# Optimization experiments

Hardware: AMD Instinct MI355X
Metric: run time of the kernel (lower is better)

Reference implementation:

```python
import jax, jax.numpy as jnp
import numpy as np
import math

D_MODEL = 1024
N_HEAD = 16
Q_DIM = K_DIM = V_DIM = 1024
SCALE = math.sqrt(D_MODEL // N_HEAD)  # 8.0
B, LQ, LK = 2, 2048, 2048


def setup_inputs() -> dict:
    key = jax.random.key(0)
    ks = jax.random.split(key, 10)
    s = 1.0 / math.sqrt(Q_DIM)
    return {
        "q": jax.random.normal(ks[0], (B, LQ, Q_DIM), jnp.float32),
        "k": jax.random.normal(ks[1], (B, LK, K_DIM), jnp.float32),
        "v": jax.random.normal(ks[2], (B, LK, V_DIM), jnp.float32),
        "mask": jax.random.randint(ks[3], (B, LQ, LK), 0, 2, jnp.int32),
        "Wq": jax.random.uniform(ks[4], (D_MODEL, Q_DIM), jnp.float32, -s, s),
        "bq": jnp.zeros((D_MODEL,), jnp.float32),
        "Wk": jax.random.uniform(ks[5], (D_MODEL, K_DIM), jnp.float32, -s, s),
        "bk": jnp.zeros((D_MODEL,), jnp.float32),
        "Wv": jax.random.uniform(ks[6], (D_MODEL, V_DIM), jnp.float32, -s, s),
        "bv": jnp.zeros((D_MODEL,), jnp.float32),
    }


def reference(q, k, v, Wq, bq, Wk, bk, Wv, bv, mask):
    b, lq, _ = q.shape
    lk = k.shape[1]
    dh = D_MODEL // N_HEAD
    # linear projections (torch Linear: x @ W.T + b)
    qh = (q @ Wq.T + bq).reshape(b, lq, N_HEAD, dh).transpose(0, 2, 1, 3)  # bhqd
    kh = (k @ Wk.T + bk).reshape(b, lk, N_HEAD, dh).transpose(0, 2, 1, 3)  # bhkd
    vh = (v @ Wv.T + bv).reshape(b, lk, N_HEAD, dh).transpose(0, 2, 1, 3)  # bhkd
    attn = jnp.einsum("bhqd,bhkd->bhqk", qh, kh) / SCALE
    m = mask[:, None, :, :]  # b1qk
    attn = jnp.where(m == 0, -jnp.inf, attn)
    # rows whose mask is all-zero are reset to 0 pre-softmax (-> uniform weights)
    row_empty = (m.sum(-1, keepdims=True) == 0)
    attn = jnp.where(row_empty, 0.0, attn)
    attn = jax.nn.softmax(attn, axis=-1)  # dropout is identity in eval mode
    v_out = jnp.einsum("bhqk,bhkd->bhqd", attn, vh)
    v_out = v_out.transpose(0, 2, 1, 3).reshape(b, lq, D_MODEL)
    k_out = jnp.einsum("bhqk,bhkd->bhqd", attn, kh)
    k_out = k_out.transpose(0, 2, 1, 3).reshape(b, lq, D_MODEL)
    return (k_out, v_out)
```

## Files before the change

### kernel.cpp

```cpp
#include <hip/hip_runtime.h>
#include <hip/hip_bf16.h>
#include <stdint.h>

typedef __bf16 bf16x8 __attribute__((ext_vector_type(8)));
typedef __bf16 bf16x4 __attribute__((ext_vector_type(4)));
typedef float f32x4 __attribute__((ext_vector_type(4)));

#define B_ 2
#define LQ_ 2048
#define LK_ 2048
#define NH_ 16
#define DH_ 64
#define DM_ 1024
#define NKT_ (LK_ / 64)

#define AS1 __attribute__((address_space(1)))
#define AS3 __attribute__((address_space(3)))

__device__ __forceinline__ void gload_lds16(const void* g, void* l) {
  __builtin_amdgcn_global_load_lds((const AS1 uint32_t*)g, (AS3 uint32_t*)l, 16, 0, 0);
}

__global__ __launch_bounds__(256) void prep_kernel(
    const float* __restrict__ q, const float* __restrict__ k,
    const float* __restrict__ v, const float* __restrict__ wq,
    const float* __restrict__ wk, const float* __restrict__ wv,
    const int* __restrict__ mask,
    __bf16* __restrict__ Xt0, __bf16* __restrict__ Xt1, __bf16* __restrict__ Xt2,
    __bf16* __restrict__ Wt0, __bf16* __restrict__ Wt1, __bf16* __restrict__ Wt2,
    unsigned* __restrict__ maskp) {
  const int t = threadIdx.x;
  const int bidx = blockIdx.x;
  if (bidx >= 960) {
    int pb = bidx - 960;
    int lane = t & 63;
    size_t gi = ((size_t)pb * 256 + t) * 4;
    int4 mv = *(const int4*)(mask + gi);
    unsigned nib = (mv.x != 0 ? 1u : 0u) | (mv.y != 0 ? 2u : 0u) |
                   (mv.z != 0 ? 4u : 0u) | (mv.w != 0 ? 8u : 0u);
    unsigned vv = nib << ((lane & 7) * 4);
    vv |= __shfl_xor(vv, 1, 64);
    vv |= __shfl_xor(vv, 2, 64);
    vv |= __shfl_xor(vv, 4, 64);
    if ((lane & 7) == 0) maskp[gi >> 5] = vv;
    return;
  }
  __shared__ __align__(16) __bf16 lb[16][1032];
  const float* src; __bf16* dst; int rows, m0;
  if (bidx < 256)      { src = q;  dst = Xt0; rows = 4096; m0 = bidx * 16; }
  else if (bidx < 512) { src = k;  dst = Xt1; rows = 4096; m0 = (bidx - 256) * 16; }
  else if (bidx < 768) { src = v;  dst = Xt2; rows = 4096; m0 = (bidx - 512) * 16; }
  else if (bidx < 832) { src = wq; dst = Wt0; rows = 1024; m0 = (bidx - 768) * 16; }
  else if (bidx < 896) { src = wk; dst = Wt1; rows = 1024; m0 = (bidx - 832) * 16; }
  else                 { src = wv; dst = Wt2; rows = 1024; m0 = (bidx - 896) * 16; }
#pragma unroll
  for (int i = 0; i < 16; i++) {
    float4 f = *(const float4*)(src + (size_t)(m0 + i) * DM_ + t * 4);
    bf16x4 o;
    o[0] = (__bf16)f.x; o[1] = (__bf16)f.y; o[2] = (__bf16)f.z; o[3] = (__bf16)f.w;
    *(bf16x4*)&lb[i][t * 4] = o;
  }
  __syncthreads();
  const int wave = t >> 6, lane = t & 63;
  const int m = lane >> 2, c = lane & 3;
#pragma unroll
  for (int j = 0; j < 8; j++) {
    int kt = wave * 8 + j;
    bf16x8 val = *(const bf16x8*)&lb[m][kt * 32 + (c ^ (m & 3)) * 8];
    *(bf16x8*)(dst + ((size_t)kt * rows + m0 + m) * 32 + c * 8) = val;
  }
}

__global__ __launch_bounds__(256) void proj_kernel(
    const __bf16* __restrict__ Xt0, const __bf16* __restrict__ Xt1,
    const __bf16* __restrict__ Xt2,
    const float* __restrict__ b0p, const float* __restrict__ b1p,
    const float* __restrict__ b2p,
    const __bf16* __restrict__ Wt0, const __bf16* __restrict__ Wt1,
    const __bf16* __restrict__ Wt2,
    __bf16* __restrict__ qh, __bf16* __restrict__ kh,
    __bf16* __restrict__ khT, __bf16* __restrict__ vhT) {
  __shared__ __align__(16) __bf16 smem[2][2][128 * 32];
  __bf16* cbuf = &smem[0][0][0];

  const int mode = blockIdx.z;
  const __bf16* Xt = mode == 0 ? Xt0 : (mode == 1 ? Xt1 : Xt2);
  const __bf16* Wt = mode == 0 ? Wt0 : (mode == 1 ? Wt1 : Wt2);
  const float* bias = mode == 0 ? b0p : (mode == 1 ? b1p : b2p);
  __bf16* ostd = mode == 0 ? qh : (mode == 1 ? kh : nullptr);
  __bf16* otr = mode == 0 ? nullptr : (mode == 1 ? khT : vhT);

  const int t = threadIdx.x;
  const int wave = t >> 6, lane = t & 63;
  const int lo16 = lane & 15, quad = lane >> 4;
  const int wm = wave >> 1, wn = wave & 1;
  const int m0 = blockIdx.x * 128, n0 = blockIdx.y * 128;

  f32x4 acc[4][4] = {};

  auto stage = [&](int kt, int sel) {
#pragma unroll
    for (int ii = 2 * wave; ii < 2 * wave + 2; ii++) {
      gload_lds16(Xt + ((size_t)kt * 4096 + m0 + ii * 16) * 32 + lane * 8,
                  &smem[sel][0][ii * 512]);
      gload_lds16(Wt + ((size_t)kt * 1024 + n0 + ii * 16) * 32 + lane * 8,
                  &smem[sel][1][ii * 512]);
    }
  };

  stage(0, 0);
  for (int kt = 0; kt < 32; kt++) {
    const int sel = kt & 1;
    __syncthreads();
    if (kt + 1 < 32) stage(kt + 1, sel ^ 1);
    bf16x8 af[4], bfr[4];
#pragma unroll
    for (int g = 0; g < 4; g++) {
      int ar = wm * 64 + g * 16 + lo16;
      af[g] = *(const bf16x8*)(&smem[sel][0][ar * 32 + (quad ^ (ar & 3)) * 8]);
      int br = wn * 64 + g * 16 + lo16;
      bfr[g] = *(const bf16x8*)(&smem[sel][1][br * 32 + (quad ^ (br & 3)) * 8]);
    }
#pragma unroll
    for (int gm = 0; gm < 4; gm++)
#pragma unroll
      for (int gn = 0; gn < 4; gn++)
        acc[gm][gn] =
            __builtin_amdgcn_mfma_f32_16x16x32_bf16(af[gm], bfr[gn], acc[gm][gn], 0, 0, 0);
  }

  const int b = m0 >> 11, l0 = m0 & 2047;
  for (int nhf = 0; nhf < 2; nhf++) {
    int h = (n0 >> 6) + nhf;
    int bh = b * NH_ + h;
    if (ostd) {
      __syncthreads();
      if (wn == nhf) {
#pragma unroll
        for (int gn = 0; gn < 4; gn++) {
          float bi = bias[n0 + nhf * 64 + gn * 16 + lo16];
#pragma unroll
          for (int gm = 0; gm < 4; gm++)
#pragma unroll
            for (int r = 0; r < 4; r++)
              cbuf[(wm * 64 + gm * 16 + quad * 4 + r) * 72 + gn * 16 + lo16] =
                  (__bf16)(acc[gm][gn][r] + bi);
        }
      }
      __syncthreads();
      int m = t >> 1, coff = (t & 1) * 32;
      __bf16* dst = ostd + ((size_t)bh * LQ_ + l0 + m) * DH_ + coff;
#pragma unroll
      for (int j = 0; j < 4; j++)
        *(bf16x8*)(dst + j * 8) = *(const bf16x8*)&cbuf[m * 72 + coff + j * 8];
    }
    if (otr) {
      __syncthreads();
      if (wn == nhf) {
#pragma unroll
        for (int gn = 0; gn < 4; gn++) {
          float bi = bias[n0 + nhf * 64 + gn * 16 + lo16];
#pragma unroll
          for (int gm = 0; gm < 4; gm++) {
            bf16x4 pk;
#pragma unroll
            for (int r = 0; r < 4; r++) pk[r] = (__bf16)(acc[gm][gn][r] + bi);
            *(bf16x4*)&cbuf[(gn * 16 + lo16) * 136 + wm * 64 + gm * 16 + quad * 4] = pk;
          }
        }
      }
      __syncthreads();
      int d = t >> 2, mc = (t & 3) * 32;
      int kti = (l0 + mc) >> 6, kl = (l0 + mc) & 63;
      __bf16* dst = otr + ((size_t)(bh * NKT_ + kti) * 64 + d) * 64 + kl;
#pragma unroll
      for (int j = 0; j < 4; j++)
        *(bf16x8*)(dst + j * 8) = *(const bf16x8*)&cbuf[d * 136 + mc + j * 8];
    }
  }
}

__global__ __launch_bounds__(256) void attn_kernel(
    const __bf16* __restrict__ qh, const __bf16* __restrict__ kh,
    const __bf16* __restrict__ khT, const __bf16* __restrict__ vhT,
    const unsigned* __restrict__ maskp,
    float* __restrict__ out_k, float* __restrict__ out_v) {
  __shared__ __align__(16) __bf16 kbuf[2][64 * 64];
  __shared__ __align__(16) __bf16 ktbuf[2][64 * 64];
  __shared__ __align__(16) __bf16 vtbuf[2][64 * 64];
  __shared__ __align__(16) __bf16 p_lds[4][2][16][72];

  const int t = threadIdx.x;
  const int wave = t >> 6, lane = t & 63;
  const int lo16 = lane & 15, quad = lane >> 4;
  const int bh = blockIdx.x;
  const int b = bh >> 4, h = bh & 15;
  const int q0 = blockIdx.y * 128 + wave * 16;
  const int srow = lane >> 3;
  const int scg = (lane & 7) ^ srow;
  const int rsw = lo16 & 7;

  bf16x8 a_q0[2], a_q1[2];
#pragma unroll
  for (int g = 0; g < 2; g++) {
    const __bf16* qrow = qh + ((size_t)bh * LQ_ + q0 + g * 64 + lo16) * DH_ + quad * 8;
    a_q0[g] = *(const bf16x8*)(qrow);
    a_q1[g] = *(const bf16x8*)(qrow + 32);
  }

  f32x4 acc_v[2][4] = {};
  f32x4 acc_k[2][4] = {};
  float lsum[2][4] = {};

  const __bf16* khb = kh + (size_t)bh * LK_ * DH_;
  const __bf16* ktb = khT + (size_t)bh * LK_ * DH_;
  const __bf16* vtb = vhT + (size_t)bh * LK_ * DH_;

  auto stage = [&](int kti, int sel) {
    const int tb = kti * 4096;
#pragma unroll
    for (int ii = 2 * wave; ii < 2 * wave + 2; ii++) {
      int row = ii * 8 + srow;
      gload_lds16(khb + (size_t)(kti * 64 + row) * DH_ + scg * 8, &kbuf[sel][ii * 512]);
      gload_lds16(ktb + tb + row * 64 + scg * 8, &ktbuf[sel][ii * 512]);
      gload_lds16(vtb + tb + row * 64 + scg * 8, &vtbuf[sel][ii * 512]);
    }
  };

  stage(0, 0);
  for (int kti = 0; kti < NKT_; kti++) {
    const int cur = kti & 1;
    __syncthreads();
    if (kti + 1 < NKT_) stage(kti + 1, cur ^ 1);

    unsigned mw[2][2][4];
#pragma unroll
    for (int g = 0; g < 2; g++) {
      const unsigned* mb =
          maskp + ((size_t)b * LQ_ + q0 + g * 64 + quad * 4) * (LK_ / 32) + kti * 2;
#pragma unroll
      for (int r = 0; r < 4; r++) {
        mw[g][0][r] = mb[r * (LK_ / 32)];
        mw[g][1][r] = mb[r * (LK_ / 32) + 1];
      }
    }

    f32x4 s[2][4];
#pragma unroll
    for (int gg = 0; gg < 4; gg++) {
      int row = gg * 16 + lo16;
      bf16x8 kb0 = *(const bf16x8*)(&kbuf[cur][row * 64 + ((quad ^ rsw) * 8)]);
      bf16x8 kb1 = *(const bf16x8*)(&kbuf[cur][row * 64 + (((quad + 4) ^ rsw) * 8)]);
#pragma unroll
      for (int g = 0; g < 2; g++) {
        f32x4 z = {};
        z = __builtin_amdgcn_mfma_f32_16x16x32_bf16(a_q0[g], kb0, z, 0, 0, 0);
        z = __builtin_amdgcn_mfma_f32_16x16x32_bf16(a_q1[g], kb1, z, 0, 0, 0);
        s[g][gg] = z;
      }
    }

#pragma unroll
    for (int g = 0; g < 2; g++)
#pragma unroll
      for (int gg = 0; gg < 4; gg++) {
        int bitpos = (gg * 16 + lo16) & 31;
#pragma unroll
        for (int r = 0; r < 4; r++) {
          unsigned w = mw[g][gg >> 1][r];
          float pe = __builtin_amdgcn_exp2f(s[g][gg][r] * 0.18033688f);
          float p = ((w >> bitpos) & 1) ? pe : 0.0f;
          s[g][gg][r] = p;
          lsum[g][r] += p;
        }
      }

#pragma unroll
    for (int g = 0; g < 2; g++)
#pragma unroll
      for (int gg = 0; gg < 4; gg++)
#pragma unroll
        for (int r = 0; r < 4; r++)
          p_lds[wave][g][quad * 4 + r][gg * 16 + lo16] = (__bf16)s[g][gg][r];
    bf16x8 a_p[2][2];
#pragma unroll
    for (int g = 0; g < 2; g++) {
      a_p[g][0] = *(const bf16x8*)&p_lds[wave][g][lo16][quad * 8];
      a_p[g][1] = *(const bf16x8*)&p_lds[wave][g][lo16][32 + quad * 8];
    }

#pragma unroll
    for (int gg = 0; gg < 4; gg++) {
      int row = gg * 16 + lo16;
      bf16x8 bv0 = *(const bf16x8*)(&vtbuf[cur][row * 64 + ((quad ^ rsw) * 8)]);
      bf16x8 bv1 = *(const bf16x8*)(&vtbuf[cur][row * 64 + (((quad + 4) ^ rsw) * 8)]);
      bf16x8 bk0 = *(const bf16x8*)(&ktbuf[cur][row * 64 + ((quad ^ rsw) * 8)]);
      bf16x8 bk1 = *(const bf16x8*)(&ktbuf[cur][row * 64 + (((quad + 4) ^ rsw) * 8)]);
#pragma unroll
      for (int g = 0; g < 2; g++) {
        acc_v[g][gg] = __builtin_amdgcn_mfma_f32_16x16x32_bf16(a_p[g][0], bv0, acc_v[g][gg], 0, 0, 0);
        acc_v[g][gg] = __builtin_amdgcn_mfma_f32_16x16x32_bf16(a_p[g][1], bv1, acc_v[g][gg], 0, 0, 0);
        acc_k[g][gg] = __builtin_amdgcn_mfma_f32_16x16x32_bf16(a_p[g][0], bk0, acc_k[g][gg], 0, 0, 0);
        acc_k[g][gg] = __builtin_amdgcn_mfma_f32_16x16x32_bf16(a_p[g][1], bk1, acc_k[g][gg], 0, 0, 0);
      }
    }
  }

#pragma unroll
  for (int off = 1; off < 16; off <<= 1) {
#pragma unroll
    for (int g = 0; g < 2; g++)
#pragma unroll
      for (int r = 0; r < 4; r++) lsum[g][r] += __shfl_xor(lsum[g][r], off, 64);
  }
#pragma unroll
  for (int g = 0; g < 2; g++) {
    float inv_l[4];
#pragma unroll
    for (int r = 0; r < 4; r++) inv_l[r] = 1.0f / lsum[g][r];
    size_t obase = ((size_t)b * LQ_ + q0 + g * 64 + quad * 4) * DM_ + h * DH_;
#pragma unroll
    for (int gg = 0; gg < 4; gg++) {
#pragma unroll
      for (int r = 0; r < 4; r++) {
        size_t idx = obase + (size_t)r * DM_ + gg * 16 + lo16;
        out_k[idx] = acc_k[g][gg][r] * inv_l[r];
        out_v[idx] = acc_v[g][gg][r] * inv_l[r];
      }
    }
  }
}

extern "C" void kernel_launch(void* const* d_in, const int* in_sizes, int n_in,
                              void* d_out, int out_size, void* d_ws, size_t ws_size,
                              hipStream_t stream) {
  const float* q = (const float*)d_in[0];
  const float* k = (const float*)d_in[1];
  const float* v = (const float*)d_in[2];
  const int* mask = (const int*)d_in[3];
  const float* Wq = (const float*)d_in[4];
  const float* bq = (const float*)d_in[5];
  const float* Wk = (const float*)d_in[6];
  const float* bk = (const float*)d_in[7];
  const float* Wv = (const float*)d_in[8];
  const float* bv = (const float*)d_in[9];
  float* out = (float*)d_out;

  const size_t HTOT = (size_t)B_ * NH_ * LQ_ * DH_;
  const size_t XTOT = (size_t)B_ * LQ_ * DM_;
  __bf16* qh = (__bf16*)d_ws;
  __bf16* kh = qh + HTOT;
  __bf16* khT = kh + HTOT;
  __bf16* vhT = khT + HTOT;
  unsigned* maskp = (unsigned*)(vhT + HTOT);

  __bf16* Xt0 = (__bf16*)d_out;
  __bf16* Xt1 = Xt0 + XTOT;
  __bf16* Xt2 = Xt1 + XTOT;
  __bf16* Wt0 = Xt2 + XTOT;
  __bf16* Wt1 = Wt0 + (size_t)DM_ * DM_;
  __bf16* Wt2 = Wt1 + (size_t)DM_ * DM_;

  prep_kernel<<<960 + 8192, 256, 0, stream>>>(
      q, k, v, Wq, Wk, Wv, mask, Xt0, Xt1, Xt2, Wt0, Wt1, Wt2, maskp);
  proj_kernel<<<dim3(32, 8, 3), 256, 0, stream>>>(
      Xt0, Xt1, Xt2, bq, bk, bv, Wt0, Wt1, Wt2, qh, kh, khT, vhT);
  attn_kernel<<<dim3(32, 16), 256, 0, stream>>>(qh, kh, khT, vhT, maskp,
                                                out, out + (size_t)B_ * LQ_ * DM_);
}
```

Baseline: 272.6 us.

## Split attention key tile across wave pairs with 512-thread blocks

```diff
diff --git a/kernel.cpp b/kernel.cpp
--- a/kernel.cpp
+++ b/kernel.cpp
@@ -89,6 +89,7 @@
   const float* bias = mode == 0 ? b0p : (mode == 1 ? b1p : b2p);
   __bf16* ostd = mode == 0 ? qh : (mode == 1 ? kh : nullptr);
   __bf16* otr = mode == 0 ? nullptr : (mode == 1 ? khT : vhT);
+  const float osc = mode == 0 ? 0.18033688f : 1.0f;
 
   const int t = threadIdx.x;
   const int wave = t >> 6, lane = t & 63;
@@ -144,7 +145,7 @@
 #pragma unroll
             for (int r = 0; r < 4; r++)
               cbuf[(wm * 64 + gm * 16 + quad * 4 + r) * 72 + gn * 16 + lo16] =
-                  (__bf16)(acc[gm][gn][r] + bi);
+                  (__bf16)((acc[gm][gn][r] + bi) * osc);
         }
       }
       __syncthreads();
@@ -180,22 +181,23 @@
   }
 }
 
-__global__ __launch_bounds__(256) void attn_kernel(
+__global__ __launch_bounds__(512) void attn_kernel(
     const __bf16* __restrict__ qh, const __bf16* __restrict__ kh,
     const __bf16* __restrict__ khT, const __bf16* __restrict__ vhT,
     const unsigned* __restrict__ maskp,
     float* __restrict__ out_k, float* __restrict__ out_v) {
-  __shared__ __align__(16) __bf16 kbuf[2][64 * 64];
-  __shared__ __align__(16) __bf16 ktbuf[2][64 * 64];
-  __shared__ __align__(16) __bf16 vtbuf[2][64 * 64];
-  __shared__ __align__(16) __bf16 p_lds[4][2][16][72];
+  __shared__ __align__(16) __bf16 tiles[3][2][64 * 64];
+  __shared__ __align__(16) __bf16 p_lds[4][32][72];
+  float* red = (float*)&tiles[0][0][0];
 
   const int t = threadIdx.x;
   const int wave = t >> 6, lane = t & 63;
   const int lo16 = lane & 15, quad = lane >> 4;
+  const int half = wave & 1;
+  const int qs = wave >> 1;
   const int bh = blockIdx.x;
   const int b = bh >> 4, h = bh & 15;
-  const int q0 = blockIdx.y * 128 + wave * 16;
+  const int q0 = blockIdx.y * 128 + qs * 32;
   const int srow = lane >> 3;
   const int scg = (lane & 7) ^ srow;
   const int rsw = lo16 & 7;
@@ -203,28 +205,29 @@
   bf16x8 a_q0[2], a_q1[2];
 #pragma unroll
   for (int g = 0; g < 2; g++) {
-    const __bf16* qrow = qh + ((size_t)bh * LQ_ + q0 + g * 64 + lo16) * DH_ + quad * 8;
+    const __bf16* qrow = qh + ((size_t)bh * LQ_ + q0 + g * 16 + lo16) * DH_ + quad * 8;
     a_q0[g] = *(const bf16x8*)(qrow);
     a_q1[g] = *(const bf16x8*)(qrow + 32);
   }
 
+  bf16x8 ones;
+#pragma unroll
+  for (int j = 0; j < 8; j++) ones[j] = (__bf16)1.0f;
+
   f32x4 acc_v[2][4] = {};
   f32x4 acc_k[2][4] = {};
-  float lsum[2][4] = {};
+  f32x4 acc_l[2] = {};
 
   const __bf16* khb = kh + (size_t)bh * LK_ * DH_;
   const __bf16* ktb = khT + (size_t)bh * LK_ * DH_;
   const __bf16* vtb = vhT + (size_t)bh * LK_ * DH_;
 
+  const int row_s = wave * 8 + srow;
   auto stage = [&](int kti, int sel) {
     const int tb = kti * 4096;
-#pragma unroll
-    for (int ii = 2 * wave; ii < 2 * wave + 2; ii++) {
-      int row = ii * 8 + srow;
-      gload_lds16(khb + (size_t)(kti * 64 + row) * DH_ + scg * 8, &kbuf[sel][ii * 512]);
-      gload_lds16(ktb + tb + row * 64 + scg * 8, &ktbuf[sel][ii * 512]);
-      gload_lds16(vtb + tb + row * 64 + scg * 8, &vtbuf[sel][ii * 512]);
-    }
+    gload_lds16(khb + (size_t)(kti * 64 + row_s) * DH_ + scg * 8, &tiles[0][sel][wave * 512]);
+    gload_lds16(ktb + tb + row_s * 64 + scg * 8, &tiles[1][sel][wave * 512]);
+    gload_lds16(vtb + tb + row_s * 64 + scg * 8, &tiles[2][sel][wave * 512]);
   };
 
   stage(0, 0);
@@ -233,99 +236,114 @@
     __syncthreads();
     if (kti + 1 < NKT_) stage(kti + 1, cur ^ 1);
 
-    unsigned mw[2][2][4];
+    unsigned mw[2][4];
 #pragma unroll
     for (int g = 0; g < 2; g++) {
       const unsigned* mb =
-          maskp + ((size_t)b * LQ_ + q0 + g * 64 + quad * 4) * (LK_ / 32) + kti * 2;
-#pragma unroll
-      for (int r = 0; r < 4; r++) {
-        mw[g][0][r] = mb[r * (LK_ / 32)];
-        mw[g][1][r] = mb[r * (LK_ / 32) + 1];
-      }
-    }
-
-    f32x4 s[2][4];
-#pragma unroll
-    for (int gg = 0; gg < 4; gg++) {
-      int row = gg * 16 + lo16;
-      bf16x8 kb0 = *(const bf16x8*)(&kbuf[cur][row * 64 + ((quad ^ rsw) * 8)]);
-      bf16x8 kb1 = *(const bf16x8*)(&kbuf[cur][row * 64 + (((quad + 4) ^ rsw) * 8)]);
+          maskp + ((size_t)b * LQ_ + q0 + g * 16 + quad * 4) * (LK_ / 32) + kti * 2 + half;
+#pragma unroll
+      for (int r = 0; r < 4; r++) mw[g][r] = mb[r * (LK_ / 32)];
+    }
+
+    f32x4 s[2][2];
+#pragma unroll
+    for (int kk = 0; kk < 2; kk++) {
+      int krow = half * 32 + kk * 16 + lo16;
+      bf16x8 kb0 = *(const bf16x8*)(&tiles[0][cur][krow * 64 + ((quad ^ rsw) * 8)]);
+      bf16x8 kb1 = *(const bf16x8*)(&tiles[0][cur][krow * 64 + (((quad + 4) ^ rsw) * 8)]);
 #pragma unroll
       for (int g = 0; g < 2; g++) {
         f32x4 z = {};
         z = __builtin_amdgcn_mfma_f32_16x16x32_bf16(a_q0[g], kb0, z, 0, 0, 0);
         z = __builtin_amdgcn_mfma_f32_16x16x32_bf16(a_q1[g], kb1, z, 0, 0, 0);
-        s[g][gg] = z;
+        s[g][kk] = z;
       }
     }
 
 #pragma unroll
     for (int g = 0; g < 2; g++)
 #pragma unroll
-      for (int gg = 0; gg < 4; gg++) {
-        int bitpos = (gg * 16 + lo16) & 31;
+      for (int kk = 0; kk < 2; kk++) {
+        int bitpos = kk * 16 + lo16;
 #pragma unroll
         for (int r = 0; r < 4; r++) {
-          unsigned w = mw[g][gg >> 1][r];
-          float pe = __builtin_amdgcn_exp2f(s[g][gg][r] * 0.18033688f);
-          float p = ((w >> bitpos) & 1) ? pe : 0.0f;
-          s[g][gg][r] = p;
-          lsum[g][r] += p;
+          float pe = __builtin_amdgcn_exp2f(s[g][kk][r]);
+          float p = ((mw[g][r] >> bitpos) & 1) ? pe : 0.0f;
+          p_lds[qs][g * 16 + quad * 4 + r][half * 32 + kk * 16 + lo16] = (__bf16)p;
         }
       }
 
+    bf16x8 a_p[2];
 #pragma unroll
     for (int g = 0; g < 2; g++)
-#pragma unroll
-      for (int gg = 0; gg < 4; gg++)
-#pragma unroll
-        for (int r = 0; r < 4; r++)
-          p_lds[wave][g][quad * 4 + r][gg * 16 + lo16] = (__bf16)s[g][gg][r];
-    bf16x8 a_p[2][2];
-#pragma unroll
-    for (int g = 0; g < 2; g++) {
-      a_p[g][0] = *(const bf16x8*)&p_lds[wave][g][lo16][quad * 8];
-      a_p[g][1] = *(const bf16x8*)&p_lds[wave][g][lo16][32 + quad * 8];
-    }
+      a_p[g] = *(const bf16x8*)&p_lds[qs][g * 16 + lo16][half * 32 + quad * 8];
 
 #pragma unroll
     for (int gg = 0; gg < 4; gg++) {
-      int row = gg * 16 + lo16;
-      bf16x8 bv0 = *(const bf16x8*)(&vtbuf[cur][row * 64 + ((quad ^ rsw) * 8)]);
-      bf16x8 bv1 = *(const bf16x8*)(&vtbuf[cur][row * 64 + (((quad + 4) ^ rsw) * 8)]);
-      bf16x8 bk0 = *(const bf16x8*)(&ktbuf[cur][row * 64 + ((quad ^ rsw) * 8)]);
-      bf16x8 bk1 = *(const bf16x8*)(&ktbuf[cur][row * 64 + (((quad + 4) ^ rsw) * 8)]);
+      int row_d = gg * 16 + lo16;
+      int ch = (half * 4 + quad) ^ rsw;
+      bf16x8 bv = *(const bf16x8*)(&tiles[2][cur][row_d * 64 + ch * 8]);
+      bf16x8 bk = *(const bf16x8*)(&tiles[1][cur][row_d * 64 + ch * 8]);
 #pragma unroll
       for (int g = 0; g < 2; g++) {
-        acc_v[g][gg] = __builtin_amdgcn_mfma_f32_16x16x32_bf16(a_p[g][0], bv0, acc_v[g][gg], 0, 0, 0);
-        acc_v[g][gg] = __builtin_amdgcn_mfma_f32_16x16x32_bf16(a_p[g][1], bv1, acc_v[g][gg], 0, 0, 0);
-        acc_k[g][gg] = __builtin_amdgcn_mfma_f32_16x16x32_bf16(a_p[g][0], bk0, acc_k[g][gg], 0, 0, 0);
-        acc_k[g][gg] = __builtin_amdgcn_mfma_f32_16x16x32_bf16(a_p[g][1], bk1, acc_k[g][gg], 0, 0, 0);
-      }
-    }
-  }
-
-#pragma unroll
-  for (int off = 1; off < 16; off <<= 1) {
+        acc_v[g][gg] = __builtin_amdgcn_mfma_f32_16x16x32_bf16(a_p[g], bv, acc_v[g][gg], 0, 0, 0);
+        acc_k[g][gg] = __builtin_amdgcn_mfma_f32_16x16x32_bf16(a_p[g], bk, acc_k[g][gg], 0, 0, 0);
+      }
+    }
 #pragma unroll
     for (int g = 0; g < 2; g++)
-#pragma unroll
-      for (int r = 0; r < 4; r++) lsum[g][r] += __shfl_xor(lsum[g][r], off, 64);
-  }
+      acc_l[g] = __builtin_amdgcn_mfma_f32_16x16x32_bf16(a_p[g], ones, acc_l[g], 0, 0, 0);
+  }
+
+  const int ridx = qs * 64 + lane;
+  f32x4* red4 = (f32x4*)red;
+  __syncthreads();
+  if (half == 1) {
+#pragma unroll
+    for (int g = 0; g < 2; g++) {
+#pragma unroll
+      for (int gg = 0; gg < 4; gg++) red4[ridx * 10 + g * 4 + gg] = acc_v[g][gg];
+      red4[ridx * 10 + 8 + g] = acc_l[g];
+    }
+  }
+  __syncthreads();
+  if (half == 0) {
+#pragma unroll
+    for (int g = 0; g < 2; g++) {
+#pragma unroll
+      for (int gg = 0; gg < 4; gg++) acc_v[g][gg] += red4[ridx * 10 + g * 4 + gg];
+      acc_l[g] += red4[ridx * 10 + 8 + g];
+    }
+#pragma unroll
+    for (int g = 0; g < 2; g++) {
+#pragma unroll
+      for (int gg = 0; gg < 4; gg++) red4[ridx * 10 + g * 4 + gg] = acc_k[g][gg];
+      red4[ridx * 10 + 8 + g] = acc_l[g];
+    }
+  }
+  __syncthreads();
+  if (half == 1) {
+#pragma unroll
+    for (int g = 0; g < 2; g++) {
+#pragma unroll
+      for (int gg = 0; gg < 4; gg++) acc_k[g][gg] += red4[ridx * 10 + g * 4 + gg];
+      acc_l[g] = red4[ridx * 10 + 8 + g];
+    }
+  }
+
+  float* outp = half ? out_k : out_v;
 #pragma unroll
   for (int g = 0; g < 2; g++) {
     float inv_l[4];
 #pragma unroll
-    for (int r = 0; r < 4; r++) inv_l[r] = 1.0f / lsum[g][r];
-    size_t obase = ((size_t)b * LQ_ + q0 + g * 64 + quad * 4) * DM_ + h * DH_;
+    for (int r = 0; r < 4; r++) inv_l[r] = 1.0f / acc_l[g][r];
+    size_t obase = ((size_t)b * LQ_ + q0 + g * 16 + quad * 4) * DM_ + h * DH_;
 #pragma unroll
     for (int gg = 0; gg < 4; gg++) {
 #pragma unroll
       for (int r = 0; r < 4; r++) {
         size_t idx = obase + (size_t)r * DM_ + gg * 16 + lo16;
-        out_k[idx] = acc_k[g][gg][r] * inv_l[r];
-        out_v[idx] = acc_v[g][gg][r] * inv_l[r];
+        outp[idx] = (half ? acc_k[g][gg][r] : acc_v[g][gg][r]) * inv_l[r];
       }
     }
   }
@@ -365,6 +383,6 @@
       q, k, v, Wq, Wk, Wv, mask, Xt0, Xt1, Xt2, Wt0, Wt1, Wt2, maskp);
   proj_kernel<<<dim3(32, 8, 3), 256, 0, stream>>>(
       Xt0, Xt1, Xt2, bq, bk, bv, Wt0, Wt1, Wt2, qh, kh, khT, vhT);
-  attn_kernel<<<dim3(32, 16), 256, 0, stream>>>(qh, kh, khT, vhT, maskp,
+  attn_kernel<<<dim3(32, 16), 512, 0, stream>>>(qh, kh, khT, vhT, maskp,
                                                 out, out + (size_t)B_ * LQ_ * DM_);
 }
```

Measured after the change: 275.6 us. No clear change (+1.1%).
